# Kernel optimization log

Hardware: AMD Instinct MI355X
Metric: run time of the kernel (lower is better)

The kernel has to match this reference:

```python
import jax, jax.numpy as jnp
import numpy as np

B, N, T, D, H = 4, 8, 512, 256, 8
DK = D // H


def _dwconv(x, w, b=None):
    # x: (BN, D, T) depthwise conv, kernel 3, padding 'same', groups=D
    y = jax.lax.conv_general_dilated(
        x, w, window_strides=(1,), padding='SAME',
        feature_group_count=x.shape[1],
        dimension_numbers=('NCH', 'OIH', 'NCH'))
    if b is not None:
        y = y + b[None, :, None]
    return y


def setup_inputs() -> dict:
    key = jax.random.key(0)
    ks = jax.random.split(key, 16)
    s = 1.0 / np.sqrt(D)
    s3 = 1.0 / np.sqrt(3 * D)
    inp = {
        'query': jax.random.normal(ks[0], (B, N, T, D), jnp.float32),
        'key': jax.random.normal(ks[1], (B, N, T, D), jnp.float32),
        'value': jax.random.normal(ks[2], (B, N, T, D), jnp.float32),
        'key_padding_mask': jax.random.randint(ks[3], (B, N, T), 0, 2, jnp.int32),
        # depthwise conv params
        'w_pos': jax.random.uniform(ks[4], (D, 1, 3), jnp.float32, -0.577, 0.577),
        'b_pos': jax.random.uniform(ks[5], (D,), jnp.float32, -0.577, 0.577),
        # physics-initialized differential operators (still learnable floats)
        'w_vel': jnp.tile(jnp.array([-1.0, 0.0, 1.0], jnp.float32)[None, None, :], (D, 1, 1)),
        'w_acc': jnp.tile(jnp.array([1.0, -2.0, 1.0], jnp.float32)[None, None, :], (D, 1, 1)),
        # fusion / projection linears (stored as (in, out))
        'Wq': jax.random.uniform(ks[6], (3 * D, D), jnp.float32, -s3, s3),
        'bq': jax.random.uniform(ks[7], (D,), jnp.float32, -s3, s3),
        'Wk': jax.random.uniform(ks[8], (3 * D, D), jnp.float32, -s3, s3),
        'bk': jax.random.uniform(ks[9], (D,), jnp.float32, -s3, s3),
        'Wv': jax.random.uniform(ks[10], (D, D), jnp.float32, -s, s),
        'bv': jax.random.uniform(ks[11], (D,), jnp.float32, -s, s),
        'Wo': jax.random.uniform(ks[12], (D, D), jnp.float32, -s, s),
        'bo': jax.random.uniform(ks[13], (D,), jnp.float32, -s, s),
    }
    return inp


def reference(query, key, value, key_padding_mask,
              w_pos, b_pos, w_vel, w_acc,
              Wq, bq, Wk, bk, Wv, bv, Wo, bo):
    b, n, t, d = query.shape
    scale = jnp.float32(1.0 / np.sqrt(DK))

    def kin_feats(x):
        xin = x.reshape(b * n, t, d).transpose(0, 2, 1)  # (BN, D, T)
        p = _dwconv(xin, w_pos, b_pos)
        v = _dwconv(xin, w_vel)
        a = _dwconv(xin, w_acc)
        return jnp.concatenate([p, v, a], axis=1).transpose(0, 2, 1)  # (BN, T, 3D)

    qc = kin_feats(query)
    kc = kin_feats(key)

    Q = (qc @ Wq + bq).reshape(b, n, t, H, DK).transpose(0, 1, 3, 2, 4)  # (B,N,H,Tq,dk)
    K = (kc @ Wk + bk).reshape(b, n, t, H, DK).transpose(0, 1, 3, 2, 4)
    V = (value @ Wv + bv).reshape(b, n, t, H, DK).transpose(0, 1, 3, 2, 4)

    scores = jnp.einsum('bnhqd,bnhkd->bnhqk', Q, K) * scale
    mask = key_padding_mask.astype(bool)[:, :, None, None, :]  # (B,N,1,1,Tk)
    scores = jnp.where(mask, jnp.float32(-1e9), scores)
    attn = jax.nn.softmax(scores, axis=-1)  # dropout is identity in eval

    ctx = jnp.einsum('bnhqk,bnhkd->bnhqd', attn, V)
    ctx = ctx.transpose(0, 1, 3, 2, 4).reshape(b, n, t, d)
    return ctx @ Wo + bo
```

## Files before the change

kernel.cpp:

```cpp
#include <hip/hip_runtime.h>
#include <math.h>


typedef __attribute__((ext_vector_type(8))) short bf16x8;
typedef __attribute__((ext_vector_type(4))) float f32x4;
typedef __attribute__((ext_vector_type(16))) float f32x16;
typedef __attribute__((ext_vector_type(4))) int i32x4;

__device__ __forceinline__ unsigned short f2bf(float f) {
    unsigned u = __float_as_uint(f);
    return (unsigned short)((u + 0x7fff + ((u >> 16) & 1)) >> 16);
}
__device__ __forceinline__ float ex2(float x) {
    float r; asm("v_exp_f32 %0, %1" : "=v"(r) : "v"(x)); return r;
}
__device__ __forceinline__ int cvtpk(float lo, float hi) {
    int r; asm("v_cvt_pk_bf16_f32 %0, %1, %2" : "=v"(r) : "v"(lo), "v"(hi)); return r;
}
__device__ __forceinline__ void gll16(const void* gsrc, const void* ldst) {
    __builtin_amdgcn_global_load_lds(
        (const __attribute__((address_space(1))) unsigned int*)gsrc,
        (__attribute__((address_space(3))) unsigned int*)ldst, 16, 0, 0);
}

#define SCL (0.17677669529663689f * 1.4426950408889634f)

#define OFF_XPQ  0u
#define OFF_XPK  8421376u
#define OFF_VB   16842752u
#define OFF_BTQ  25231360u
#define OFF_BTK  25624576u
#define OFF_BEFF 26017792u
#define OFF_WVT  26019840u
#define OFF_WOT  26150912u
#define OFF_QB   26413056u
#define OFF_KB   34801664u
#define OFF_VV   43190272u
#define OFF_CTX  51578880u

__global__ __launch_bounds__(256) void cvtprep(
    const float* __restrict__ q, const float* __restrict__ k, const float* __restrict__ v,
    unsigned short* __restrict__ xpq, unsigned short* __restrict__ xpk,
    unsigned short* __restrict__ vb,
    const float* __restrict__ Wq, const float* __restrict__ Wk,
    const float* __restrict__ bq, const float* __restrict__ bk,
    const float* __restrict__ wp, const float* __restrict__ wv,
    const float* __restrict__ wa, const float* __restrict__ b_pos,
    const float* __restrict__ Wv, const float* __restrict__ Wo,
    unsigned short* __restrict__ BtQ, unsigned short* __restrict__ BtK,
    float* __restrict__ beff, unsigned short* __restrict__ WVT,
    unsigned short* __restrict__ WOT)
{
    int bid = blockIdx.x;
    if (bid < 4112) {
        int idx = bid * 256 + threadIdx.x;
        int which = idx / 526336;
        int r = idx - which * 526336;
        int bn = r / 16448;
        int rr = r - bn * 16448;
        int p = rr >> 5;
        int c8 = (rr & 31) * 8;
        const float* src = which ? k : q;
        unsigned short* dst = which ? xpk : xpq;
        unsigned o[4] = {0, 0, 0, 0};
        if (p != 0 && p != 513) {
            const float* s = src + ((size_t)(bn * 512 + p - 1) * 256 + c8);
            float4 a = *(const float4*)s;
            float4 b = *(const float4*)(s + 4);
            o[0] = f2bf(a.x) | ((unsigned)f2bf(a.y) << 16);
            o[1] = f2bf(a.z) | ((unsigned)f2bf(a.w) << 16);
            o[2] = f2bf(b.x) | ((unsigned)f2bf(b.y) << 16);
            o[3] = f2bf(b.z) | ((unsigned)f2bf(b.w) << 16);
        }
        unsigned* d = (unsigned*)(dst + ((size_t)(bn * 514 + p) * 256 + c8));
        d[0] = o[0]; d[1] = o[1]; d[2] = o[2]; d[3] = o[3];
    } else if (bid < 6160) {
        int idx = (bid - 4112) * 256 + threadIdx.x;
        int row = idx >> 5;
        int c8 = (idx & 31) * 8;
        const float* s = v + ((size_t)row * 256 + c8);
        float4 a = *(const float4*)s;
        float4 b = *(const float4*)(s + 4);
        unsigned* d = (unsigned*)(vb + ((size_t)row * 256 + c8));
        d[0] = f2bf(a.x) | ((unsigned)f2bf(a.y) << 16);
        d[1] = f2bf(a.z) | ((unsigned)f2bf(a.w) << 16);
        d[2] = f2bf(b.x) | ((unsigned)f2bf(b.y) << 16);
        d[3] = f2bf(b.z) | ((unsigned)f2bf(b.w) << 16);
    } else if (bid < 7696) {
        int idx = (bid - 6160) * 256 + threadIdx.x;
        int which = idx / 196608;
        int r = idx - which * 196608;
        int j = r >> 16;
        int rem = r & 65535;
        int n = rem >> 8;
        int d = rem & 255;
        const float* W = which ? Wk : Wq;
        float val = wp[d * 3 + j] * W[d * 256 + n]
                  + wv[d * 3 + j] * W[(256 + d) * 256 + n]
                  + wa[d * 3 + j] * W[(512 + d) * 256 + n];
        if (!which) val *= SCL;
        (which ? BtK : BtQ)[n * 768 + j * 256 + d] = f2bf(val);
    } else if (bid < 8208) {
        int idx = (bid - 7696) * 256 + threadIdx.x;
        int which = idx >> 16;
        int r = idx & 65535;
        int n = r >> 8, kk = r & 255;
        if (!which) WVT[n * 256 + kk] = f2bf(Wv[kk * 256 + n]);
        else        WOT[n * 256 + kk] = f2bf(Wo[kk * 256 + n]);
    } else {
        int which = bid - 8208;
        int n = threadIdx.x;
        const float* W = which ? Wk : Wq;
        const float* bb = which ? bk : bq;
        float s = bb[n];
        for (int d = 0; d < 256; ++d) s = fmaf(b_pos[d], W[d * 256 + n], s);
        if (!which) s *= SCL;
        beff[which * 256 + n] = s;
    }
}

template<int KTOT, bool IM2COL, typename OutT>
__device__ __forceinline__ void gemm97(
    const unsigned short* __restrict__ A, const unsigned short* __restrict__ Bt,
    const float* __restrict__ bias, OutT* __restrict__ Out,
    unsigned short* As, unsigned short* Bs)
{
    const int tid = threadIdx.x;
    const int wid = tid >> 6, l = tid & 63;
    const int l31 = l & 31, h2 = l >> 5;
    const int wm = wid >> 1, wn = wid & 1;
    const int m0 = blockIdx.x * 128, n0 = blockIdx.y * 128;

    f32x16 acc[2][2] = {};

    for (int k0 = 0; k0 < KTOT; k0 += 64) {
        __syncthreads();
        #pragma unroll
        for (int q = 0; q < 4; ++q) {
            int cidx = q * 256 + wid * 64 + l;
            int row = cidx >> 3;
            int csrc = ((cidx & 7) ^ (row & 7)) * 8;
            const unsigned short* asrc;
            if constexpr (IM2COL) {
                int seq = m0 >> 9, t0 = m0 & 511;
                asrc = A + ((size_t)(seq * 514 + t0 + row + (k0 >> 8)) * 256 + (k0 & 255) + csrc);
            } else {
                asrc = A + ((size_t)(m0 + row) * 256 + (k0 & 255) + csrc);
            }
            gll16(asrc, As + (q * 256 + wid * 64) * 8);
            gll16(Bt + (size_t)(n0 + row) * KTOT + k0 + csrc, Bs + (q * 256 + wid * 64) * 8);
        }
        __syncthreads();
        #pragma unroll
        for (int ks = 0; ks < 4; ++ks) {
            bf16x8 af[2], bfr[2];
            #pragma unroll
            for (int mt = 0; mt < 2; ++mt) {
                int r = wm * 64 + mt * 32 + l31;
                af[mt] = *(const bf16x8*)&As[r * 64 + (((ks * 2 + h2) ^ (r & 7)) * 8)];
            }
            #pragma unroll
            for (int nt = 0; nt < 2; ++nt) {
                int rn = wn * 64 + nt * 32 + l31;
                bfr[nt] = *(const bf16x8*)&Bs[rn * 64 + (((ks * 2 + h2) ^ (rn & 7)) * 8)];
            }
            #pragma unroll
            for (int mt = 0; mt < 2; ++mt)
                #pragma unroll
                for (int nt = 0; nt < 2; ++nt)
                    acc[mt][nt] = __builtin_amdgcn_mfma_f32_32x32x16_bf16(af[mt], bfr[nt], acc[mt][nt], 0, 0, 0);
        }
    }

    #pragma unroll
    for (int nt = 0; nt < 2; ++nt) {
        const int col = n0 + wn * 64 + nt * 32 + l31;
        const float bb = bias[col];
        #pragma unroll
        for (int mt = 0; mt < 2; ++mt) {
            #pragma unroll
            for (int r = 0; r < 16; ++r) {
                const int row = m0 + wm * 64 + mt * 32 + 4 * h2 + (r & 3) + 8 * (r >> 2);
                float v = acc[mt][nt][r] + bb;
                if constexpr (sizeof(OutT) == 2) Out[(size_t)row * 256 + col] = (OutT)f2bf(v);
                else Out[(size_t)row * 256 + col] = v;
            }
        }
    }
}

__global__ __launch_bounds__(256) void proj_fused(
    const unsigned short* __restrict__ XPQ, const unsigned short* __restrict__ XPK,
    const unsigned short* __restrict__ VB,
    const unsigned short* __restrict__ BTQ, const unsigned short* __restrict__ BTK,
    const unsigned short* __restrict__ WVT,
    const float* __restrict__ BEFF, const float* __restrict__ bv,
    unsigned short* __restrict__ QB, unsigned short* __restrict__ KB,
    unsigned short* __restrict__ VV)
{
    __shared__ alignas(16) unsigned short As[8192];
    __shared__ alignas(16) unsigned short Bs[8192];
    const int z = blockIdx.z;
    if (z == 0)      gemm97<768, true, unsigned short>(XPQ, BTQ, BEFF, QB, As, Bs);
    else if (z == 1) gemm97<768, true, unsigned short>(XPK, BTK, BEFF + 256, KB, As, Bs);
    else             gemm97<256, false, unsigned short>(VB, WVT, bv, VV, As, Bs);
}

__global__ __launch_bounds__(256) void outproj(
    const unsigned short* __restrict__ CTX, const unsigned short* __restrict__ WOT,
    const float* __restrict__ bo, float* __restrict__ Out)
{
    __shared__ alignas(16) unsigned short As[8192];
    __shared__ alignas(16) unsigned short Bs[8192];
    gemm97<256, false, float>(CTX, WOT, bo, Out, As, Bs);
}

__global__ __launch_bounds__(512) void attn_mfma(const unsigned short* __restrict__ Qb,
                                                 const unsigned short* __restrict__ Kb,
                                                 const unsigned short* __restrict__ Vv,
                                                 const int* __restrict__ mask,
                                                 unsigned short* __restrict__ ctx) {
    __shared__ alignas(16) unsigned short Qs[512 * 32];
    __shared__ alignas(16) unsigned short Ks[2][128 * 32];
    __shared__ alignas(16) unsigned short VsT[2][32 * 136];
    __shared__ float Mb[2][128];

    const int bnh = blockIdx.x;
    const int bn = bnh >> 3, h = bnh & 7;
    const int tid = threadIdx.x, wid = tid >> 6, l = tid & 63;
    const int g = l >> 4, r15 = l & 15;
    const unsigned short* Qg = Qb + (size_t)bn * 512 * 256 + h * 32;
    const unsigned short* Kg = Kb + (size_t)bn * 512 * 256 + h * 32;
    const unsigned short* Vg = Vv + (size_t)bn * 512 * 256 + h * 32;
    const int* mp = mask + bn * 512;
    const int srow = tid >> 2;
    const int vkey = tid & 127, vd0 = (tid >> 7) * 8;

    auto stageK = [&](int k0, int b) {
        int csrc = (((tid & 3) ^ (srow & 3))) * 8;
        gll16(Kg + ((size_t)(k0 + srow)) * 256 + csrc, &Ks[b][wid * 512]);
    };

    #pragma unroll
    for (int q = 0; q < 4; ++q) {
        int chunk = q * 512 + tid;
        int row = chunk >> 2, c = chunk & 3;
        gll16(Qg + (size_t)row * 256 + c * 8, Qs + (q * 512 + wid * 64) * 8);
    }
    stageK(0, 0);
    {
        i32x4 vr = *(const i32x4*)(const void*)(Vg + (size_t)vkey * 256 + vd0);
        #pragma unroll
        for (int i = 0; i < 4; ++i) {
            unsigned u = (unsigned)vr[i];
            VsT[0][(vd0 + 2 * i) * 136 + vkey] = (unsigned short)(u & 0xffff);
            VsT[0][(vd0 + 2 * i + 1) * 136 + vkey] = (unsigned short)(u >> 16);
        }
        if (tid < 128) Mb[0][tid] = (mp[tid] != 0) ? -1e9f : 0.f;
    }
    __syncthreads();

    bf16x8 bq[4];
    #pragma unroll
    for (int qt = 0; qt < 4; ++qt)
        bq[qt] = *(const bf16x8*)&Qs[(qt * 128 + wid * 16 + r15) * 32 + g * 8];

    float mrun[4], lrun[4];
    f32x4 accO[4][2] = {};
    #pragma unroll
    for (int qt = 0; qt < 4; ++qt) { mrun[qt] = -1e30f; lrun[qt] = 0.f; }

    for (int kt = 0; kt < 4; ++kt) {
        const int cur = kt & 1, nxt = cur ^ 1;
        const int k0n = kt * 128 + 128;

        i32x4 vr;
        int mraw = 0;
        if (kt < 3) {
            stageK(k0n, nxt);
            vr = *(const i32x4*)(const void*)(Vg + ((size_t)(k0n + vkey)) * 256 + vd0);
            if (tid < 128) mraw = mp[k0n + tid];
        }

        bf16x8 av[2][4];
        #pragma unroll
        for (int mt = 0; mt < 2; ++mt)
            #pragma unroll
            for (int s = 0; s < 4; ++s)
                av[mt][s] = *(const bf16x8*)&VsT[cur][(mt * 16 + r15) * 136 + 32 * s + 8 * g];

        #pragma unroll
        for (int qt = 0; qt < 4; ++qt) {
            float p[8][4];
            float rmax = -3e38f;
            __builtin_amdgcn_s_setprio(1);
            #pragma unroll
            for (int t2 = 0; t2 < 8; ++t2) {
                const int base = 32 * (t2 >> 1) + 4 * (t2 & 1);
                const int arow = base + 8 * (r15 >> 2) + (r15 & 3);
                bf16x8 ak = *(const bf16x8*)&Ks[cur][arow * 32 + ((g ^ (arow & 3)) * 8)];
                f32x4 cin = *(const f32x4*)&Mb[cur][base + 8 * g];
                f32x4 st = __builtin_amdgcn_mfma_f32_16x16x32_bf16(ak, bq[qt], cin, 0, 0, 0);
                #pragma unroll
                for (int r = 0; r < 4; ++r) p[t2][r] = st[r];
                rmax = fmaxf(rmax, fmaxf(fmaxf(st[0], st[1]), fmaxf(st[2], st[3])));
            }
            __builtin_amdgcn_s_setprio(0);
            rmax = fmaxf(rmax, __shfl_xor(rmax, 16, 64));
            rmax = fmaxf(rmax, __shfl_xor(rmax, 32, 64));

            if (__ballot(rmax > mrun[qt])) {
                float mnew = fmaxf(mrun[qt], rmax);
                float fs = ex2(mrun[qt] - mnew);
                lrun[qt] *= fs;
                accO[qt][0] *= fs;
                accO[qt][1] *= fs;
                mrun[qt] = mnew;
            }
            float psum = 0.f;
            #pragma unroll
            for (int t2 = 0; t2 < 8; ++t2)
                #pragma unroll
                for (int r = 0; r < 4; ++r) {
                    float e = ex2(p[t2][r] - mrun[qt]);
                    p[t2][r] = e;
                    psum += e;
                }
            psum += __shfl_xor(psum, 16, 64);
            psum += __shfl_xor(psum, 32, 64);
            lrun[qt] += psum;

            bf16x8 pb[4];
            #pragma unroll
            for (int s = 0; s < 4; ++s) {
                i32x4 bi = {cvtpk(p[2 * s][0], p[2 * s][1]), cvtpk(p[2 * s][2], p[2 * s][3]),
                            cvtpk(p[2 * s + 1][0], p[2 * s + 1][1]), cvtpk(p[2 * s + 1][2], p[2 * s + 1][3])};
                pb[s] = __builtin_bit_cast(bf16x8, bi);
            }

            __builtin_amdgcn_s_setprio(1);
            #pragma unroll
            for (int mt = 0; mt < 2; ++mt)
                #pragma unroll
                for (int s = 0; s < 4; ++s)
                    accO[qt][mt] = __builtin_amdgcn_mfma_f32_16x16x32_bf16(av[mt][s], pb[s], accO[qt][mt], 0, 0, 0);
            __builtin_amdgcn_s_setprio(0);
        }

        if (kt < 3) {
            #pragma unroll
            for (int i = 0; i < 4; ++i) {
                unsigned u = (unsigned)vr[i];
                VsT[nxt][(vd0 + 2 * i) * 136 + vkey] = (unsigned short)(u & 0xffff);
                VsT[nxt][(vd0 + 2 * i + 1) * 136 + vkey] = (unsigned short)(u >> 16);
            }
            if (tid < 128) Mb[nxt][tid] = (mraw != 0) ? -1e9f : 0.f;
        }
        __syncthreads();
    }

    #pragma unroll
    for (int qt = 0; qt < 4; ++qt) {
        const float inv = 1.f / lrun[qt];
        const size_t orow = (size_t)bn * 512 + qt * 128 + wid * 16 + r15;
        #pragma unroll
        for (int mt = 0; mt < 2; ++mt) {
            ushort4 o;
            o.x = f2bf(accO[qt][mt][0] * inv);
            o.y = f2bf(accO[qt][mt][1] * inv);
            o.z = f2bf(accO[qt][mt][2] * inv);
            o.w = f2bf(accO[qt][mt][3] * inv);
            *(ushort4*)&ctx[orow * 256 + h * 32 + mt * 16 + 4 * g] = o;
        }
    }
}

extern "C" void kernel_launch(void* const* d_in, const int* in_sizes, int n_in,
                              void* d_out, int out_size, void* d_ws, size_t ws_size,
                              hipStream_t stream) {
    const float* query = (const float*)d_in[0];
    const float* key   = (const float*)d_in[1];
    const float* value = (const float*)d_in[2];
    const int*   kpm   = (const int*)d_in[3];
    const float* w_pos = (const float*)d_in[4];
    const float* b_pos = (const float*)d_in[5];
    const float* w_vel = (const float*)d_in[6];
    const float* w_acc = (const float*)d_in[7];
    const float* Wq    = (const float*)d_in[8];
    const float* bq    = (const float*)d_in[9];
    const float* Wk    = (const float*)d_in[10];
    const float* bk    = (const float*)d_in[11];
    const float* Wv    = (const float*)d_in[12];
    const float* bv    = (const float*)d_in[13];
    const float* Wo    = (const float*)d_in[14];
    const float* bo    = (const float*)d_in[15];

    unsigned char* w = (unsigned char*)d_ws;
    unsigned short* XPQ = (unsigned short*)(w + OFF_XPQ);
    unsigned short* XPK = (unsigned short*)(w + OFF_XPK);
    unsigned short* VB  = (unsigned short*)(w + OFF_VB);
    unsigned short* BTQ = (unsigned short*)(w + OFF_BTQ);
    unsigned short* BTK = (unsigned short*)(w + OFF_BTK);
    float*          BEFF= (float*)(w + OFF_BEFF);
    unsigned short* WVT = (unsigned short*)(w + OFF_WVT);
    unsigned short* WOT = (unsigned short*)(w + OFF_WOT);
    unsigned short* QB  = (unsigned short*)(w + OFF_QB);
    unsigned short* KB  = (unsigned short*)(w + OFF_KB);
    unsigned short* VV  = (unsigned short*)(w + OFF_VV);
    unsigned short* CTX = (unsigned short*)(w + OFF_CTX);

    cvtprep<<<8210, 256, 0, stream>>>(query, key, value, XPQ, XPK, VB,
                                      Wq, Wk, bq, bk, w_pos, w_vel, w_acc, b_pos,
                                      Wv, Wo, BTQ, BTK, BEFF, WVT, WOT);

    proj_fused<<<dim3(128, 2, 3), 256, 0, stream>>>(XPQ, XPK, VB, BTQ, BTK, WVT,
                                                    BEFF, bv, QB, KB, VV);

    attn_mfma<<<256, 512, 0, stream>>>(QB, KB, VV, kpm, CTX);

    outproj<<<dim3(128, 2), 256, 0, stream>>>(CTX, WOT, bo, (float*)d_out);
}
```

Baseline: 88.21 us.

## Fuse fp32-to-bf16 conversion and im2col padding into projection GEMM loads

```diff
diff --git a/kernel.cpp b/kernel.cpp
--- a/kernel.cpp
+++ b/kernel.cpp
@@ -11,6 +11,9 @@
     unsigned u = __float_as_uint(f);
     return (unsigned short)((u + 0x7fff + ((u >> 16) & 1)) >> 16);
 }
+__device__ __forceinline__ float bf2f(unsigned short h) {
+    return __uint_as_float(((unsigned)h) << 16);
+}
 __device__ __forceinline__ float ex2(float x) {
     float r; asm("v_exp_f32 %0, %1" : "=v"(r) : "v"(x)); return r;
 }
@@ -25,9 +28,7 @@
 
 #define SCL (0.17677669529663689f * 1.4426950408889634f)
 
-#define OFF_XPQ  0u
-#define OFF_XPK  8421376u
-#define OFF_VB   16842752u
+#define OFF_ZERO 0u
 #define OFF_BTQ  25231360u
 #define OFF_BTK  25624576u
 #define OFF_BEFF 26017792u
@@ -38,10 +39,7 @@
 #define OFF_VV   43190272u
 #define OFF_CTX  51578880u
 
-__global__ __launch_bounds__(256) void cvtprep(
-    const float* __restrict__ q, const float* __restrict__ k, const float* __restrict__ v,
-    unsigned short* __restrict__ xpq, unsigned short* __restrict__ xpk,
-    unsigned short* __restrict__ vb,
+__global__ __launch_bounds__(256) void prep(
     const float* __restrict__ Wq, const float* __restrict__ Wk,
     const float* __restrict__ bq, const float* __restrict__ bk,
     const float* __restrict__ wp, const float* __restrict__ wv,
@@ -49,45 +47,11 @@
     const float* __restrict__ Wv, const float* __restrict__ Wo,
     unsigned short* __restrict__ BtQ, unsigned short* __restrict__ BtK,
     float* __restrict__ beff, unsigned short* __restrict__ WVT,
-    unsigned short* __restrict__ WOT)
+    unsigned short* __restrict__ WOT, float* __restrict__ zeropage)
 {
     int bid = blockIdx.x;
-    if (bid < 4112) {
+    if (bid < 1536) {
         int idx = bid * 256 + threadIdx.x;
-        int which = idx / 526336;
-        int r = idx - which * 526336;
-        int bn = r / 16448;
-        int rr = r - bn * 16448;
-        int p = rr >> 5;
-        int c8 = (rr & 31) * 8;
-        const float* src = which ? k : q;
-        unsigned short* dst = which ? xpk : xpq;
-        unsigned o[4] = {0, 0, 0, 0};
-        if (p != 0 && p != 513) {
-            const float* s = src + ((size_t)(bn * 512 + p - 1) * 256 + c8);
-            float4 a = *(const float4*)s;
-            float4 b = *(const float4*)(s + 4);
-            o[0] = f2bf(a.x) | ((unsigned)f2bf(a.y) << 16);
-            o[1] = f2bf(a.z) | ((unsigned)f2bf(a.w) << 16);
-            o[2] = f2bf(b.x) | ((unsigned)f2bf(b.y) << 16);
-            o[3] = f2bf(b.z) | ((unsigned)f2bf(b.w) << 16);
-        }
-        unsigned* d = (unsigned*)(dst + ((size_t)(bn * 514 + p) * 256 + c8));
-        d[0] = o[0]; d[1] = o[1]; d[2] = o[2]; d[3] = o[3];
-    } else if (bid < 6160) {
-        int idx = (bid - 4112) * 256 + threadIdx.x;
-        int row = idx >> 5;
-        int c8 = (idx & 31) * 8;
-        const float* s = v + ((size_t)row * 256 + c8);
-        float4 a = *(const float4*)s;
-        float4 b = *(const float4*)(s + 4);
-        unsigned* d = (unsigned*)(vb + ((size_t)row * 256 + c8));
-        d[0] = f2bf(a.x) | ((unsigned)f2bf(a.y) << 16);
-        d[1] = f2bf(a.z) | ((unsigned)f2bf(a.w) << 16);
-        d[2] = f2bf(b.x) | ((unsigned)f2bf(b.y) << 16);
-        d[3] = f2bf(b.z) | ((unsigned)f2bf(b.w) << 16);
-    } else if (bid < 7696) {
-        int idx = (bid - 6160) * 256 + threadIdx.x;
         int which = idx / 196608;
         int r = idx - which * 196608;
         int j = r >> 16;
@@ -100,15 +64,15 @@
                   + wa[d * 3 + j] * W[(512 + d) * 256 + n];
         if (!which) val *= SCL;
         (which ? BtK : BtQ)[n * 768 + j * 256 + d] = f2bf(val);
-    } else if (bid < 8208) {
-        int idx = (bid - 7696) * 256 + threadIdx.x;
+    } else if (bid < 2048) {
+        int idx = (bid - 1536) * 256 + threadIdx.x;
         int which = idx >> 16;
         int r = idx & 65535;
         int n = r >> 8, kk = r & 255;
         if (!which) WVT[n * 256 + kk] = f2bf(Wv[kk * 256 + n]);
         else        WOT[n * 256 + kk] = f2bf(Wo[kk * 256 + n]);
-    } else {
-        int which = bid - 8208;
+    } else if (bid < 2050) {
+        int which = bid - 2048;
         int n = threadIdx.x;
         const float* W = which ? Wk : Wq;
         const float* bb = which ? bk : bq;
@@ -116,10 +80,94 @@
         for (int d = 0; d < 256; ++d) s = fmaf(b_pos[d], W[d * 256 + n], s);
         if (!which) s *= SCL;
         beff[which * 256 + n] = s;
-    }
-}
-
-template<int KTOT, bool IM2COL, typename OutT>
+    } else {
+        if (threadIdx.x < 64) zeropage[threadIdx.x] = 0.f;
+    }
+}
+
+template<int KTOT, bool IM2COL>
+__device__ __forceinline__ void gemmf32(
+    const float* __restrict__ A, const unsigned short* __restrict__ Bt,
+    const float* __restrict__ bias, const float* __restrict__ zeropage,
+    unsigned short* __restrict__ Out, float* Asf, unsigned short* Bs)
+{
+    const int tid = threadIdx.x;
+    const int wid = tid >> 6, l = tid & 63;
+    const int l31 = l & 31, h2 = l >> 5;
+    const int wm = wid >> 1, wn = wid & 1;
+    const int m0 = blockIdx.x * 128, n0 = blockIdx.y * 128;
+
+    f32x16 acc[2][2] = {};
+
+    for (int k0 = 0; k0 < KTOT; k0 += 64) {
+        __syncthreads();
+        #pragma unroll
+        for (int q = 0; q < 8; ++q) {
+            int cidx = q * 256 + tid;
+            int row = cidx >> 4, cch = cidx & 15;
+            int csrc = (cch ^ (row & 15)) * 4;
+            const float* asrc;
+            if constexpr (IM2COL) {
+                int seq = m0 >> 9, t0 = m0 & 511;
+                int st = t0 + row + (k0 >> 8) - 1;
+                asrc = (st >= 0 && st < 512)
+                     ? A + ((size_t)(seq * 512 + st) * 256 + (k0 & 255) + csrc)
+                     : zeropage + csrc;
+            } else {
+                asrc = A + ((size_t)(m0 + row) * 256 + k0 + csrc);
+            }
+            gll16(asrc, Asf + (size_t)cidx * 4);
+        }
+        #pragma unroll
+        for (int q = 0; q < 4; ++q) {
+            int cidx = q * 256 + tid;
+            int row = cidx >> 3, c = cidx & 7;
+            gll16(Bt + (size_t)(n0 + row) * KTOT + k0 + ((c ^ (row & 7)) * 8),
+                  Bs + cidx * 8);
+        }
+        __syncthreads();
+        #pragma unroll
+        for (int ks = 0; ks < 4; ++ks) {
+            const int c = ks * 2 + h2;
+            bf16x8 af[2], bfr[2];
+            #pragma unroll
+            for (int mt = 0; mt < 2; ++mt) {
+                int r = wm * 64 + mt * 32 + l31;
+                f32x4 f0 = *(const f32x4*)&Asf[r * 64 + (((2 * c) ^ (r & 15)) * 4)];
+                f32x4 f1 = *(const f32x4*)&Asf[r * 64 + (((2 * c + 1) ^ (r & 15)) * 4)];
+                i32x4 w = {cvtpk(f0[0], f0[1]), cvtpk(f0[2], f0[3]),
+                           cvtpk(f1[0], f1[1]), cvtpk(f1[2], f1[3])};
+                af[mt] = __builtin_bit_cast(bf16x8, w);
+            }
+            #pragma unroll
+            for (int nt = 0; nt < 2; ++nt) {
+                int rn = wn * 64 + nt * 32 + l31;
+                bfr[nt] = *(const bf16x8*)&Bs[rn * 64 + ((c ^ (rn & 7)) * 8)];
+            }
+            #pragma unroll
+            for (int mt = 0; mt < 2; ++mt)
+                #pragma unroll
+                for (int nt = 0; nt < 2; ++nt)
+                    acc[mt][nt] = __builtin_amdgcn_mfma_f32_32x32x16_bf16(af[mt], bfr[nt], acc[mt][nt], 0, 0, 0);
+        }
+    }
+
+    #pragma unroll
+    for (int nt = 0; nt < 2; ++nt) {
+        const int col = n0 + wn * 64 + nt * 32 + l31;
+        const float bb = bias[col];
+        #pragma unroll
+        for (int mt = 0; mt < 2; ++mt) {
+            #pragma unroll
+            for (int r = 0; r < 16; ++r) {
+                const int row = m0 + wm * 64 + mt * 32 + 4 * h2 + (r & 3) + 8 * (r >> 2);
+                Out[(size_t)row * 256 + col] = f2bf(acc[mt][nt][r] + bb);
+            }
+        }
+    }
+}
+
+template<int KTOT, typename OutT>
 __device__ __forceinline__ void gemm97(
     const unsigned short* __restrict__ A, const unsigned short* __restrict__ Bt,
     const float* __restrict__ bias, OutT* __restrict__ Out,
@@ -137,18 +185,11 @@
         __syncthreads();
         #pragma unroll
         for (int q = 0; q < 4; ++q) {
-            int cidx = q * 256 + wid * 64 + l;
+            int cidx = q * 256 + tid;
             int row = cidx >> 3;
             int csrc = ((cidx & 7) ^ (row & 7)) * 8;
-            const unsigned short* asrc;
-            if constexpr (IM2COL) {
-                int seq = m0 >> 9, t0 = m0 & 511;
-                asrc = A + ((size_t)(seq * 514 + t0 + row + (k0 >> 8)) * 256 + (k0 & 255) + csrc);
-            } else {
-                asrc = A + ((size_t)(m0 + row) * 256 + (k0 & 255) + csrc);
-            }
-            gll16(asrc, As + (q * 256 + wid * 64) * 8);
-            gll16(Bt + (size_t)(n0 + row) * KTOT + k0 + csrc, Bs + (q * 256 + wid * 64) * 8);
+            gll16(A + (size_t)(m0 + row) * 256 + (k0 & 255) + csrc, As + (size_t)cidx * 8);
+            gll16(Bt + (size_t)(n0 + row) * KTOT + k0 + csrc, Bs + (size_t)cidx * 8);
         }
         __syncthreads();
         #pragma unroll
@@ -190,20 +231,21 @@
 }
 
 __global__ __launch_bounds__(256) void proj_fused(
-    const unsigned short* __restrict__ XPQ, const unsigned short* __restrict__ XPK,
-    const unsigned short* __restrict__ VB,
+    const float* __restrict__ query, const float* __restrict__ key,
+    const float* __restrict__ value,
     const unsigned short* __restrict__ BTQ, const unsigned short* __restrict__ BTK,
     const unsigned short* __restrict__ WVT,
     const float* __restrict__ BEFF, const float* __restrict__ bv,
+    const float* __restrict__ zeropage,
     unsigned short* __restrict__ QB, unsigned short* __restrict__ KB,
     unsigned short* __restrict__ VV)
 {
-    __shared__ alignas(16) unsigned short As[8192];
+    __shared__ alignas(16) float Asf[8192];
     __shared__ alignas(16) unsigned short Bs[8192];
     const int z = blockIdx.z;
-    if (z == 0)      gemm97<768, true, unsigned short>(XPQ, BTQ, BEFF, QB, As, Bs);
-    else if (z == 1) gemm97<768, true, unsigned short>(XPK, BTK, BEFF + 256, KB, As, Bs);
-    else             gemm97<256, false, unsigned short>(VB, WVT, bv, VV, As, Bs);
+    if (z == 0)      gemmf32<768, true>(query, BTQ, BEFF, zeropage, QB, Asf, Bs);
+    else if (z == 1) gemmf32<768, true>(key, BTK, BEFF + 256, zeropage, KB, Asf, Bs);
+    else             gemmf32<256, false>(value, WVT, bv, zeropage, VV, Asf, Bs);
 }
 
 __global__ __launch_bounds__(256) void outproj(
@@ -212,7 +254,7 @@
 {
     __shared__ alignas(16) unsigned short As[8192];
     __shared__ alignas(16) unsigned short Bs[8192];
-    gemm97<256, false, float>(CTX, WOT, bo, Out, As, Bs);
+    gemm97<256, float>(CTX, WOT, bo, Out, As, Bs);
 }
 
 __global__ __launch_bounds__(512) void attn_mfma(const unsigned short* __restrict__ Qb,
@@ -396,9 +438,7 @@
     const float* bo    = (const float*)d_in[15];
 
     unsigned char* w = (unsigned char*)d_ws;
-    unsigned short* XPQ = (unsigned short*)(w + OFF_XPQ);
-    unsigned short* XPK = (unsigned short*)(w + OFF_XPK);
-    unsigned short* VB  = (unsigned short*)(w + OFF_VB);
+    float*          ZP  = (float*)(w + OFF_ZERO);
     unsigned short* BTQ = (unsigned short*)(w + OFF_BTQ);
     unsigned short* BTK = (unsigned short*)(w + OFF_BTK);
     float*          BEFF= (float*)(w + OFF_BEFF);
@@ -409,12 +449,11 @@
     unsigned short* VV  = (unsigned short*)(w + OFF_VV);
     unsigned short* CTX = (unsigned short*)(w + OFF_CTX);
 
-    cvtprep<<<8210, 256, 0, stream>>>(query, key, value, XPQ, XPK, VB,
-                                      Wq, Wk, bq, bk, w_pos, w_vel, w_acc, b_pos,
-                                      Wv, Wo, BTQ, BTK, BEFF, WVT, WOT);
-
-    proj_fused<<<dim3(128, 2, 3), 256, 0, stream>>>(XPQ, XPK, VB, BTQ, BTK, WVT,
-                                                    BEFF, bv, QB, KB, VV);
+    prep<<<2051, 256, 0, stream>>>(Wq, Wk, bq, bk, w_pos, w_vel, w_acc, b_pos,
+                                   Wv, Wo, BTQ, BTK, BEFF, WVT, WOT, ZP);
+
+    proj_fused<<<dim3(128, 2, 3), 256, 0, stream>>>(query, key, value, BTQ, BTK, WVT,
+                                                    BEFF, bv, ZP, QB, KB, VV);
 
     attn_mfma<<<256, 512, 0, stream>>>(QB, KB, VV, kpm, CTX);
 
```

Result: faster. 80.77 us (-8.4%).
